# Kernel optimization log

Hardware: AMD Instinct MI355X
Metric: run time of the kernel (lower is better)

Reference implementation:

```python
import jax, jax.numpy as jnp
import numpy as np
from jax import lax

K = 5        # kernel_size
KN = 32      # kernel_num
C_IN = 16
PRIOR_VAR = 0.01


def _extract_patches(x, k):
    # TF tf.image.extract_patches VALID, stride 1: last-dim order is (kh, kw, c)
    B, H, W, C = x.shape
    Ho, Wo = H - k + 1, W - k + 1
    p = jnp.stack([x[:, i:i + Ho, j:j + Wo, :] for i in range(k) for j in range(k)], axis=3)
    return p.reshape(B, Ho * Wo, k * k * C)  # [B, P, k*k*C]


def setup_inputs() -> dict:
    key = jax.random.key(0)
    k1, k2, k3, k4 = jax.random.split(key, 4)
    mu_in = jax.random.normal(k1, (32, 64, 64, C_IN), dtype=jnp.float32)
    Sigma_in = jax.random.uniform(k2, (32, 64, 64, C_IN), dtype=jnp.float32)
    # GlorotNormal for w_mu
    fan_in = K * K * C_IN
    fan_out = K * K * KN
    std = jnp.sqrt(2.0 / (fan_in + fan_out)).astype(jnp.float32)
    w_mu = jax.random.normal(k3, (K, K, C_IN, KN), dtype=jnp.float32) * std
    w_sigma = jax.random.uniform(k4, (KN,), dtype=jnp.float32, minval=-4.6, maxval=-2.25)
    return {"mu_in": mu_in, "Sigma_in": Sigma_in, "w_mu": w_mu, "w_sigma": w_sigma}


def reference(mu_in, Sigma_in, w_mu, w_sigma):
    B = mu_in.shape[0]
    # KL regularizer (broadcast w_sigma over w_mu shape, mean over all)
    kl_loss = (jnp.log(PRIOR_VAR) - 1.0 - w_sigma
               + jax.nn.softplus(w_sigma) / PRIOR_VAR
               + jnp.square(w_mu) / PRIOR_VAR)
    kl_conv = 0.5 * jnp.mean(kl_loss)

    w_sigma_2 = jax.nn.softplus(w_sigma)  # [KN]

    # mean path: standard conv
    mu_out = lax.conv_general_dilated(
        mu_in, w_mu, window_strides=(1, 1), padding='VALID',
        dimension_numbers=('NHWC', 'HWIO', 'NHWC'))  # [B, Ho, Wo, KN]
    Ho = mu_out.shape[1]

    mu_dim = jnp.float32(K * K * C_IN)

    diag_sigma_g = _extract_patches(Sigma_in, K)          # [B, P, D]
    mu_in_patches = _extract_patches(mu_in, K)            # [B, P, D]

    mu_cov_square = jnp.square(w_mu).reshape(K * K * C_IN, KN)
    mu_wT_sigmags_mu_w = diag_sigma_g @ (mu_cov_square / mu_dim)          # [B, P, KN]
    trace = jnp.sum(diag_sigma_g, axis=2, keepdims=True) * w_sigma_2 / mu_dim  # [B, P, KN]
    mu_gT_mu_g = jnp.sum(jnp.square(mu_in_patches), axis=-1, keepdims=True)    # [B, P, 1]
    sigmaw_mu_gT_mu_g = mu_gT_mu_g * w_sigma_2 / mu_dim                   # [B, P, KN]

    Sigma_out = trace + mu_wT_sigmags_mu_w + sigmaw_mu_gT_mu_g
    Sigma_out = jax.nn.softplus(Sigma_out.reshape(B, Ho, Ho, KN))
    return mu_out, Sigma_out, kl_conv
```

## Files before the change

kernel.cpp:

```cpp
#include <hip/hip_runtime.h>
#include <hip/hip_bf16.h>
#include <math.h>

#define KK 5
#define KN 32
#define CIN 16
#define H 64
#define W 64
#define NB 32
#define HO 60
#define WO 60
#define D_TOT 400
#define OUT_PLANE (NB*HO*WO*KN)

#define TH 8
#define TW 16
#define IN_R 12
#define IN_C 20
#define CPAD 24
#define TILE_SH (IN_R*IN_C*CPAD)
#define NKSTEP 13

typedef short short8 __attribute__((ext_vector_type(8)));
typedef float f32x4 __attribute__((ext_vector_type(4)));

__device__ __forceinline__ ushort f2bf(float x) {
    __hip_bfloat16 h = __float2bfloat16(x);
    return *reinterpret_cast<ushort*>(&h);
}
__device__ __forceinline__ float bf2f(ushort u) {
    __hip_bfloat16 h = *reinterpret_cast<__hip_bfloat16*>(&u);
    return __bfloat162float(h);
}
__device__ __forceinline__ float softplusf(float x) {
    return (x > 20.0f) ? x : __logf(1.0f + __expf(x));
}

__global__ void prep_all(const float* __restrict__ w_mu, const float* __restrict__ w_sigma,
                         ushort* __restrict__ bmu, ushort* __restrict__ bsq,
                         float* __restrict__ spw, float* __restrict__ kl_out) {
    __shared__ float red[256];
    int t = threadIdx.x;
    if (blockIdx.x < 52) {
        int idx = blockIdx.x * 256 + t;
        int j  = idx & 7;
        int l  = (idx >> 3) & 63;
        int nt = (idx >> 9) & 1;
        int ts = idx >> 10;
        int k  = ts * 32 + ((l >> 4) & 3) * 8 + j;
        int n  = nt * 16 + (l & 15);
        float w = (k < D_TOT) ? w_mu[k * KN + n] : 0.0f;
        bmu[idx] = f2bf(w);
        bsq[idx] = f2bf(w * w * (1.0f / 400.0f));
    } else {
        float s = 0.f;
        for (int i = t; i < D_TOT * KN; i += 256) { float w = w_mu[i]; s += w * w; }
        red[t] = s;
        __syncthreads();
        for (int off = 128; off > 0; off >>= 1) {
            if (t < off) red[t] += red[t + off];
            __syncthreads();
        }
        float sum_w2 = red[0];
        if (t < KN) {
            float ws = w_sigma[t];
            spw[t] = log1pf(expf(ws)) * (1.0f / 400.0f);
        }
        if (t == 0) {
            float sws = 0.f;
            for (int kn = 0; kn < KN; ++kn) {
                float ws = w_sigma[kn];
                float sp = log1pf(expf(ws));
                sws += -ws + sp * 100.0f;
            }
            float kl = 0.5f * (-4.605170186f - 1.0f + sws * (1.0f / 32.0f)
                               + sum_w2 * (100.0f / 12800.0f));
            *kl_out = kl;
        }
    }
}

__global__ __launch_bounds__(256, 4)
void vdp_main(const float* __restrict__ mu_in, const float* __restrict__ sig_in,
              const ushort* __restrict__ bmu_g, const ushort* __restrict__ bsq_g,
              const float* __restrict__ spw,
              float* __restrict__ mu_out, float* __restrict__ sig_out) {
    __shared__ ushort tiles[2 * TILE_SH + 8];
    __shared__ float csum[IN_R * IN_C];
    __shared__ float t12s[TH * TW];

    const int b   = blockIdx.z;
    const int ho0 = blockIdx.y * TH;
    const int wo0 = blockIdx.x * TW;
    const int t   = threadIdx.x;

    if (t < 8) tiles[2 * TILE_SH + t] = 0;

    for (int i = t; i < IN_R * IN_C * 4; i += 256) {
        int row = i / 80;
        int rem = i - row * 80;
        int col = rem >> 2, c4 = rem & 3;
        int gh = ho0 + row, gw = wo0 + col;
        float4 vm = make_float4(0.f, 0.f, 0.f, 0.f), vs = vm;
        if (gh < H && gw < W) {
            size_t g = (((size_t)b * H + gh) * W + gw) * CIN + c4 * 4;
            vm = *(const float4*)(mu_in + g);
            vs = *(const float4*)(sig_in + g);
        }
        int sb = (row * IN_C + col) * CPAD + c4 * 4;
        ushort4 um, us;
        um.x = f2bf(vm.x); um.y = f2bf(vm.y); um.z = f2bf(vm.z); um.w = f2bf(vm.w);
        us.x = f2bf(vs.x); us.y = f2bf(vs.y); us.z = f2bf(vs.z); us.w = f2bf(vs.w);
        *(ushort4*)&tiles[sb] = um;
        *(ushort4*)&tiles[TILE_SH + sb] = us;
    }
    __syncthreads();

    if (t < IN_R * IN_C) {
        int sb = t * CPAD;
        float acc = 0.f;
#pragma unroll
        for (int g = 0; g < 4; ++g) {
            ushort4 m4 = *(ushort4*)&tiles[sb + g * 4];
            ushort4 s4 = *(ushort4*)&tiles[TILE_SH + sb + g * 4];
            float m0 = bf2f(m4.x), m1 = bf2f(m4.y), m2 = bf2f(m4.z), m3 = bf2f(m4.w);
            acc += bf2f(s4.x) + bf2f(s4.y) + bf2f(s4.z) + bf2f(s4.w);
            acc += m0 * m0 + m1 * m1 + m2 * m2 + m3 * m3;
        }
        csum[t] = acc;
    }
    __syncthreads();

    if (t < TH * TW) {
        int r = t >> 4, c = t & 15;
        float s = 0.f;
#pragma unroll
        for (int kh = 0; kh < KK; ++kh)
#pragma unroll
            for (int kw = 0; kw < KK; ++kw)
                s += csum[(r + kh) * IN_C + c + kw];
        t12s[t] = s;
    }
    __syncthreads();

    const int w    = t >> 6;
    const int l    = t & 63;
    const int col  = l & 15;
    const int q    = l >> 4;
    const int qh   = q >> 1;
    const int qc   = q & 1;

    const char* lds = (const char*)tiles;
    int base0 = ((2 * w + 0) * IN_C + col) * (CPAD * 2) + qc * 16;
    int base1 = ((2 * w + 1) * IN_C + col) * (CPAD * 2) + qc * 16;
    const int qh48  = qh * 48;
    const int qh768 = qh * 768;
    const int zpad  = 2 * TILE_SH * 2;

    const short8* Bmu8 = (const short8*)bmu_g;
    const short8* Bsq8 = (const short8*)bsq_g;

    f32x4 accm[2][2], accs[2][2];
    f32x4 z = {0.f, 0.f, 0.f, 0.f};
#pragma unroll
    for (int a = 0; a < 2; ++a)
#pragma unroll
        for (int bn = 0; bn < 2; ++bn) { accm[a][bn] = z; accs[a][bn] = z; }

    constexpr int F0v[NKSTEP]  = {0, 2, 4, 21, 23, 40, 42, 44, 61, 63, 80, 82, 84};
    constexpr int D16[NKSTEP] = {0, 0, 1, 0, 0, 0, 0, 1, 0, 0, 0, 0, 2};

#pragma unroll
    for (int ts = 0; ts < NKSTEP; ++ts) {
        short8 am0, am1, as0, as1;
        if (D16[ts] == 2) {
            int a0 = qh ? zpad : (base0 + F0v[ts] * 48);
            int a1 = qh ? zpad : (base1 + F0v[ts] * 48);
            am0 = *(const short8*)(lds + a0);
            am1 = *(const short8*)(lds + a1);
            as0 = *(const short8*)(lds + a0 + (qh ? 0 : TILE_SH * 2));
            as1 = *(const short8*)(lds + a1 + (qh ? 0 : TILE_SH * 2));
        } else {
            int ex = (D16[ts] ? qh768 : qh48) + F0v[ts] * 48;
            am0 = *(const short8*)(lds + base0 + ex);
            am1 = *(const short8*)(lds + base1 + ex);
            as0 = *(const short8*)(lds + TILE_SH * 2 + base0 + ex);
            as1 = *(const short8*)(lds + TILE_SH * 2 + base1 + ex);
        }
        short8 bm0 = Bmu8[(ts * 2 + 0) * 64 + l];
        short8 bm1 = Bmu8[(ts * 2 + 1) * 64 + l];
        short8 bs0 = Bsq8[(ts * 2 + 0) * 64 + l];
        short8 bs1 = Bsq8[(ts * 2 + 1) * 64 + l];

        accm[0][0] = __builtin_amdgcn_mfma_f32_16x16x32_bf16(am0, bm0, accm[0][0], 0, 0, 0);
        accm[0][1] = __builtin_amdgcn_mfma_f32_16x16x32_bf16(am0, bm1, accm[0][1], 0, 0, 0);
        accm[1][0] = __builtin_amdgcn_mfma_f32_16x16x32_bf16(am1, bm0, accm[1][0], 0, 0, 0);
        accm[1][1] = __builtin_amdgcn_mfma_f32_16x16x32_bf16(am1, bm1, accm[1][1], 0, 0, 0);
        accs[0][0] = __builtin_amdgcn_mfma_f32_16x16x32_bf16(as0, bs0, accs[0][0], 0, 0, 0);
        accs[0][1] = __builtin_amdgcn_mfma_f32_16x16x32_bf16(as0, bs1, accs[0][1], 0, 0, 0);
        accs[1][0] = __builtin_amdgcn_mfma_f32_16x16x32_bf16(as1, bs0, accs[1][0], 0, 0, 0);
        accs[1][1] = __builtin_amdgcn_mfma_f32_16x16x32_bf16(as1, bs1, accs[1][1], 0, 0, 0);
    }

    float spw0 = spw[col], spw1 = spw[16 + col];
#pragma unroll
    for (int mt = 0; mt < 2; ++mt) {
        int ho = ho0 + 2 * w + mt;
        if (ho >= HO) continue;
#pragma unroll
        for (int reg = 0; reg < 4; ++reg) {
            int wo = wo0 + q * 4 + reg;
            if (wo >= WO) continue;
            float t12v = t12s[(2 * w + mt) * TW + q * 4 + reg];
            size_t base = (((size_t)b * HO + ho) * WO + wo) * KN;
            mu_out[base + col]      = accm[mt][0][reg];
            mu_out[base + 16 + col] = accm[mt][1][reg];
            float s0 = accs[mt][0][reg] + t12v * spw0;
            float s1 = accs[mt][1][reg] + t12v * spw1;
            sig_out[base + col]      = softplusf(s0);
            sig_out[base + 16 + col] = softplusf(s1);
        }
    }
}

extern "C" void kernel_launch(void* const* d_in, const int* in_sizes, int n_in,
                              void* d_out, int out_size, void* d_ws, size_t ws_size,
                              hipStream_t stream) {
    const float* mu_in   = (const float*)d_in[0];
    const float* sig_in  = (const float*)d_in[1];
    const float* w_mu    = (const float*)d_in[2];
    const float* w_sigma = (const float*)d_in[3];

    float* out     = (float*)d_out;
    float* mu_out  = out;
    float* sig_out = out + (size_t)OUT_PLANE;
    float* kl_out  = out + 2 * (size_t)OUT_PLANE;

    ushort* bmu = (ushort*)d_ws;
    ushort* bsq = bmu + 13312;
    float*  spw = (float*)(bsq + 13312);

    prep_all<<<53, 256, 0, stream>>>(w_mu, w_sigma, bmu, bsq, spw, kl_out);
    vdp_main<<<dim3(4, 8, NB), 256, 0, stream>>>(mu_in, sig_in, bmu, bsq, spw,
                                                 mu_out, sig_out);
}
```

Baseline: 112.5 us.

## Shrink output tile to 4 rows per block, one M-tile per wave, nontemporal stores

Halves the tile height so each wave computes a single 16-wide output row instead of two, with the grid raised from 8 to 15 row-blocks. Because 60 is divisible by 4, the row bounds checks are dropped. The change also packs bf16 conversion with a paired intrinsic, uses nontemporal stores for the outputs and raises the occupancy hint. It is meant to cut wasted rows and LDS per block and raise occupancy, at the cost of more halo reloading, since each block now loads 8 input rows to produce 4 output rows.

After: 120.1 us. 6.8% more time.

```diff
diff --git a/kernel.cpp b/kernel.cpp
--- a/kernel.cpp
+++ b/kernel.cpp
@@ -13,9 +13,9 @@
 #define D_TOT 400
 #define OUT_PLANE (NB*HO*WO*KN)
 
-#define TH 8
+#define TH 4
 #define TW 16
-#define IN_R 12
+#define IN_R 8
 #define IN_C 20
 #define CPAD 24
 #define TILE_SH (IN_R*IN_C*CPAD)
@@ -31,6 +31,14 @@
 __device__ __forceinline__ float bf2f(ushort u) {
     __hip_bfloat16 h = *reinterpret_cast<__hip_bfloat16*>(&u);
     return __bfloat162float(h);
+}
+__device__ __forceinline__ ushort4 pk4(float4 v) {
+    union { __hip_bfloat162 h; ushort2 u; } a, b;
+    a.h = __float22bfloat162_rn(make_float2(v.x, v.y));
+    b.h = __float22bfloat162_rn(make_float2(v.z, v.w));
+    ushort4 r;
+    r.x = a.u.x; r.y = a.u.y; r.z = b.u.x; r.w = b.u.y;
+    return r;
 }
 __device__ __forceinline__ float softplusf(float x) {
     return (x > 20.0f) ? x : __logf(1.0f + __expf(x));
@@ -80,7 +88,7 @@
     }
 }
 
-__global__ __launch_bounds__(256, 4)
+__global__ __launch_bounds__(256, 5)
 void vdp_main(const float* __restrict__ mu_in, const float* __restrict__ sig_in,
               const ushort* __restrict__ bmu_g, const ushort* __restrict__ bsq_g,
               const float* __restrict__ spw,
@@ -100,19 +108,16 @@
         int row = i / 80;
         int rem = i - row * 80;
         int col = rem >> 2, c4 = rem & 3;
-        int gh = ho0 + row, gw = wo0 + col;
+        int gw = wo0 + col;
         float4 vm = make_float4(0.f, 0.f, 0.f, 0.f), vs = vm;
-        if (gh < H && gw < W) {
-            size_t g = (((size_t)b * H + gh) * W + gw) * CIN + c4 * 4;
+        if (gw < W) {
+            size_t g = (((size_t)b * H + ho0 + row) * W + gw) * CIN + c4 * 4;
             vm = *(const float4*)(mu_in + g);
             vs = *(const float4*)(sig_in + g);
         }
         int sb = (row * IN_C + col) * CPAD + c4 * 4;
-        ushort4 um, us;
-        um.x = f2bf(vm.x); um.y = f2bf(vm.y); um.z = f2bf(vm.z); um.w = f2bf(vm.w);
-        us.x = f2bf(vs.x); us.y = f2bf(vs.y); us.z = f2bf(vs.z); us.w = f2bf(vs.w);
-        *(ushort4*)&tiles[sb] = um;
-        *(ushort4*)&tiles[TILE_SH + sb] = us;
+        *(ushort4*)&tiles[sb] = pk4(vm);
+        *(ushort4*)&tiles[TILE_SH + sb] = pk4(vs);
     }
     __syncthreads();
 
@@ -151,75 +156,59 @@
     const int qc   = q & 1;
 
     const char* lds = (const char*)tiles;
-    int base0 = ((2 * w + 0) * IN_C + col) * (CPAD * 2) + qc * 16;
-    int base1 = ((2 * w + 1) * IN_C + col) * (CPAD * 2) + qc * 16;
+    const int base  = (w * IN_C + col) * (CPAD * 2) + qc * 16;
     const int qh48  = qh * 48;
     const int qh768 = qh * 768;
     const int zpad  = 2 * TILE_SH * 2;
+    const int SGOFF = TILE_SH * 2;
 
     const short8* Bmu8 = (const short8*)bmu_g;
     const short8* Bsq8 = (const short8*)bsq_g;
 
-    f32x4 accm[2][2], accs[2][2];
+    f32x4 accm[2], accs[2];
     f32x4 z = {0.f, 0.f, 0.f, 0.f};
-#pragma unroll
-    for (int a = 0; a < 2; ++a)
-#pragma unroll
-        for (int bn = 0; bn < 2; ++bn) { accm[a][bn] = z; accs[a][bn] = z; }
-
-    constexpr int F0v[NKSTEP]  = {0, 2, 4, 21, 23, 40, 42, 44, 61, 63, 80, 82, 84};
+    accm[0] = z; accm[1] = z; accs[0] = z; accs[1] = z;
+
+    constexpr int F0v[NKSTEP] = {0, 2, 4, 21, 23, 40, 42, 44, 61, 63, 80, 82, 84};
     constexpr int D16[NKSTEP] = {0, 0, 1, 0, 0, 0, 0, 1, 0, 0, 0, 0, 2};
 
 #pragma unroll
     for (int ts = 0; ts < NKSTEP; ++ts) {
-        short8 am0, am1, as0, as1;
+        short8 am, as;
         if (D16[ts] == 2) {
-            int a0 = qh ? zpad : (base0 + F0v[ts] * 48);
-            int a1 = qh ? zpad : (base1 + F0v[ts] * 48);
-            am0 = *(const short8*)(lds + a0);
-            am1 = *(const short8*)(lds + a1);
-            as0 = *(const short8*)(lds + a0 + (qh ? 0 : TILE_SH * 2));
-            as1 = *(const short8*)(lds + a1 + (qh ? 0 : TILE_SH * 2));
+            int a0 = qh ? zpad : (base + F0v[ts] * 48);
+            am = *(const short8*)(lds + a0);
+            as = *(const short8*)(lds + a0 + (qh ? 0 : SGOFF));
         } else {
             int ex = (D16[ts] ? qh768 : qh48) + F0v[ts] * 48;
-            am0 = *(const short8*)(lds + base0 + ex);
-            am1 = *(const short8*)(lds + base1 + ex);
-            as0 = *(const short8*)(lds + TILE_SH * 2 + base0 + ex);
-            as1 = *(const short8*)(lds + TILE_SH * 2 + base1 + ex);
+            am = *(const short8*)(lds + base + ex);
+            as = *(const short8*)(lds + SGOFF + base + ex);
         }
         short8 bm0 = Bmu8[(ts * 2 + 0) * 64 + l];
         short8 bm1 = Bmu8[(ts * 2 + 1) * 64 + l];
         short8 bs0 = Bsq8[(ts * 2 + 0) * 64 + l];
         short8 bs1 = Bsq8[(ts * 2 + 1) * 64 + l];
 
-        accm[0][0] = __builtin_amdgcn_mfma_f32_16x16x32_bf16(am0, bm0, accm[0][0], 0, 0, 0);
-        accm[0][1] = __builtin_amdgcn_mfma_f32_16x16x32_bf16(am0, bm1, accm[0][1], 0, 0, 0);
-        accm[1][0] = __builtin_amdgcn_mfma_f32_16x16x32_bf16(am1, bm0, accm[1][0], 0, 0, 0);
-        accm[1][1] = __builtin_amdgcn_mfma_f32_16x16x32_bf16(am1, bm1, accm[1][1], 0, 0, 0);
-        accs[0][0] = __builtin_amdgcn_mfma_f32_16x16x32_bf16(as0, bs0, accs[0][0], 0, 0, 0);
-        accs[0][1] = __builtin_amdgcn_mfma_f32_16x16x32_bf16(as0, bs1, accs[0][1], 0, 0, 0);
-        accs[1][0] = __builtin_amdgcn_mfma_f32_16x16x32_bf16(as1, bs0, accs[1][0], 0, 0, 0);
-        accs[1][1] = __builtin_amdgcn_mfma_f32_16x16x32_bf16(as1, bs1, accs[1][1], 0, 0, 0);
-    }
-
-    float spw0 = spw[col], spw1 = spw[16 + col];
-#pragma unroll
-    for (int mt = 0; mt < 2; ++mt) {
-        int ho = ho0 + 2 * w + mt;
-        if (ho >= HO) continue;
-#pragma unroll
-        for (int reg = 0; reg < 4; ++reg) {
-            int wo = wo0 + q * 4 + reg;
-            if (wo >= WO) continue;
-            float t12v = t12s[(2 * w + mt) * TW + q * 4 + reg];
-            size_t base = (((size_t)b * HO + ho) * WO + wo) * KN;
-            mu_out[base + col]      = accm[mt][0][reg];
-            mu_out[base + 16 + col] = accm[mt][1][reg];
-            float s0 = accs[mt][0][reg] + t12v * spw0;
-            float s1 = accs[mt][1][reg] + t12v * spw1;
-            sig_out[base + col]      = softplusf(s0);
-            sig_out[base + 16 + col] = softplusf(s1);
-        }
+        accm[0] = __builtin_amdgcn_mfma_f32_16x16x32_bf16(am, bm0, accm[0], 0, 0, 0);
+        accm[1] = __builtin_amdgcn_mfma_f32_16x16x32_bf16(am, bm1, accm[1], 0, 0, 0);
+        accs[0] = __builtin_amdgcn_mfma_f32_16x16x32_bf16(as, bs0, accs[0], 0, 0, 0);
+        accs[1] = __builtin_amdgcn_mfma_f32_16x16x32_bf16(as, bs1, accs[1], 0, 0, 0);
+    }
+
+    const float spw0 = spw[col], spw1 = spw[16 + col];
+    const int ho = ho0 + w;
+#pragma unroll
+    for (int reg = 0; reg < 4; ++reg) {
+        int wo = wo0 + q * 4 + reg;
+        if (wo >= WO) continue;
+        float t12v = t12s[w * TW + q * 4 + reg];
+        size_t basep = (((size_t)b * HO + ho) * WO + wo) * KN;
+        __builtin_nontemporal_store(accm[0][reg], mu_out + basep + col);
+        __builtin_nontemporal_store(accm[1][reg], mu_out + basep + 16 + col);
+        float s0 = accs[0][reg] + t12v * spw0;
+        float s1 = accs[1][reg] + t12v * spw1;
+        __builtin_nontemporal_store(softplusf(s0), sig_out + basep + col);
+        __builtin_nontemporal_store(softplusf(s1), sig_out + basep + 16 + col);
     }
 }
 
@@ -241,6 +230,6 @@
     float*  spw = (float*)(bsq + 13312);
 
     prep_all<<<53, 256, 0, stream>>>(w_mu, w_sigma, bmu, bsq, spw, kl_out);
-    vdp_main<<<dim3(4, 8, NB), 256, 0, stream>>>(mu_in, sig_in, bmu, bsq, spw,
-                                                 mu_out, sig_out);
-}
+    vdp_main<<<dim3(4, 15, NB), 256, 0, stream>>>(mu_in, sig_in, bmu, bsq, spw,
+                                                  mu_out, sig_out);
+}
```
